# Performance work log

Measured on AMD Instinct MI355X. Metric: run time of the kernel, lower is better.

## Reference

```python
import jax, jax.numpy as jnp
import numpy as np


def setup_inputs() -> dict:
    key = jax.random.key(0)
    k1, k2, k3 = jax.random.split(key, 3)
    N, C_in, H, W = 32, 16, 256, 256
    C_out, K = 64, 3
    x = jax.random.normal(k1, (N, C_in, H, W), dtype=jnp.float32)
    # match nn.Conv2d default init scale roughly (values irrelevant for correctness harness)
    fan_in = C_in * K * K
    bound = 1.0 / np.sqrt(fan_in)
    conv_weight = jax.random.normal(k2, (C_out, C_in, K, K), dtype=jnp.float32) * bound
    conv_bias = jax.random.normal(k3, (C_out,), dtype=jnp.float32) * bound
    return {"x": x, "conv_weight": conv_weight, "conv_bias": conv_bias}


def reference(x, conv_weight, conv_bias):
    # Conv2d: stride=1, padding=0 (VALID), dilation=1, groups=1
    y = jax.lax.conv_general_dilated(
        x, conv_weight,
        window_strides=(1, 1), padding='VALID',
        dimension_numbers=('NCHW', 'OIHW', 'NCHW'),
    ) + conv_bias[None, :, None, None]          # (N, C_out, OH, OW)
    y = jnp.min(y, axis=1, keepdims=True)       # min over output channels -> (N, 1, OH, OW)
    return jnp.tanh(jnp.tanh(y))                # double tanh
```

## Files before the change

kernel.cpp:

```cpp
#include <hip/hip_runtime.h>
#include <hip/hip_bf16.h>

typedef __attribute__((ext_vector_type(8)))  short short8;
typedef __attribute__((ext_vector_type(4)))  float f32x4;
typedef __attribute__((ext_vector_type(16))) float f32x16;

#define CIN   16
#define HH    256
#define WW    256
#define OHH   254
#define OWW   254

#define HSTR   (36 * 8)
#define HALF   (34 * HSTR + 8)

__device__ __forceinline__ ushort f2bf(float f) {
    unsigned u = __builtin_bit_cast(unsigned, f);
    unsigned r = (u + 0x7fffu + ((u >> 16) & 1u)) >> 16;
    return (ushort)r;
}

__device__ __forceinline__ float dtanh2(float x) {
    const float K = 2.8853900817779268f;
    float xc = fminf(fmaxf(x, -9.0f), 9.0f);
    float e1 = __builtin_amdgcn_exp2f(K * xc);
    float t1 = 1.0f - 2.0f * __builtin_amdgcn_rcpf(e1 + 1.0f);
    float e2 = __builtin_amdgcn_exp2f(K * t1);
    return 1.0f - 2.0f * __builtin_amdgcn_rcpf(e2 + 1.0f);
}

__global__ void prep_weights(const float* __restrict__ wsrc, ushort* __restrict__ wfrag) {
    int idx = blockIdx.x * 256 + threadIdx.x;
    if (idx >= 9216) return;
    int r    = idx & 7;
    int lane = (idx >> 3) & 63;
    int j    = (idx >> 9) & 1;
    int tap  = idx >> 10;
    int ci   = 8 * (lane >> 5) + r;
    int co   = j * 32 + (lane & 31);
    int kh   = tap / 3, kw = tap - 3 * kh;
    wfrag[idx] = f2bf(wsrc[(co * CIN + ci) * 9 + kh * 3 + kw]);
}

__global__ __launch_bounds__(256, 4) void conv_min_tanh(
        const float* __restrict__ x, const ushort* __restrict__ wfrag,
        const float* __restrict__ bias, float* __restrict__ out) {
    __shared__ ushort lds[2 * HALF];

    const int tid = threadIdx.x;
    const int n   = blockIdx.z;
    const int oh0 = blockIdx.y * 32;
    const int ow0 = blockIdx.x * 32;
    const int HW  = HH * WW;

    const float* xb = x + (size_t)n * CIN * HW;
    auto stage_pos = [&](int pos) {
        int hp  = pos / 36;
        int r2  = pos - hp * 36;
        int ciq = r2 / 9;
        int w4  = r2 - ciq * 9;
        int hg  = min(oh0 + hp, HH - 1);
        int wg  = min(ow0 + 4 * w4, WW - 4);
        const float* src = xb + (size_t)(ciq * 4) * HW + hg * WW + wg;
        f32x4 v0 = *reinterpret_cast<const f32x4*>(src);
        f32x4 v1 = *reinterpret_cast<const f32x4*>(src + HW);
        f32x4 v2 = *reinterpret_cast<const f32x4*>(src + 2 * HW);
        f32x4 v3 = *reinterpret_cast<const f32x4*>(src + 3 * HW);
        ushort* dst = &lds[(ciq >> 1) * HALF + (hp * 36 + 4 * w4) * 8 + (ciq & 1) * 4];
#pragma unroll
        for (int e = 0; e < 4; ++e) {
            unsigned lo, hi;
            asm("v_cvt_pk_bf16_f32 %0, %1, %2" : "=v"(lo) : "v"(v0[e]), "v"(v1[e]));
            asm("v_cvt_pk_bf16_f32 %0, %1, %2" : "=v"(hi) : "v"(v2[e]), "v"(v3[e]));
            uint2 pk; pk.x = lo; pk.y = hi;
            *reinterpret_cast<uint2*>(dst + e * 8) = pk;
        }
    };
#pragma unroll
    for (int it = 0; it < 4; ++it) stage_pos(tid + it * 256);
    if (tid < 1224 - 1024) stage_pos(tid + 1024);

    const int lane  = tid & 63;
    const int wid   = tid >> 6;
    const int jw    = wid & 1;
    const int rh    = wid >> 1;
    const int px    = lane & 31;
    const int khalf = lane >> 5;

    short8 wf[9];
#pragma unroll
    for (int tap = 0; tap < 9; ++tap)
        wf[tap] = *reinterpret_cast<const short8*>(wfrag + ((tap * 2 + jw) * 64 + lane) * 8);
    f32x16 bi;
#pragma unroll
    for (int q4 = 0; q4 < 4; ++q4) {
        f32x4 b = *reinterpret_cast<const f32x4*>(bias + jw * 32 + 4 * khalf + 8 * q4);
#pragma unroll
        for (int s = 0; s < 4; ++s) bi[q4 * 4 + s] = b[s];
    }
    const ushort* bp[9];
#pragma unroll
    for (int tap = 0; tap < 9; ++tap) {
        int kh = tap / 3, kw = tap - 3 * kh;
        bp[tap] = &lds[khalf * HALF + (rh * 16 + kh) * HSTR + (px + kw) * 8];
    }

    __syncthreads();

    float mv[16];
#pragma unroll
    for (int i = 0; i < 16; ++i) {
        f32x16 a = bi;
#pragma unroll
        for (int tap = 0; tap < 9; ++tap) {
            short8 b = *reinterpret_cast<const short8*>(bp[tap] + i * HSTR);
            a = __builtin_amdgcn_mfma_f32_32x32x16_bf16(wf[tap], b, a, 0, 0, 0);
        }
        float v = a[0];
#pragma unroll
        for (int r = 1; r < 16; ++r) v = fminf(v, a[r]);
        v = fminf(v, __shfl_xor(v, 32, 64));
        mv[i] = v;
    }

    __syncthreads();

    if (lane < 32) {
#pragma unroll
        for (int i = 0; i < 16; ++i)
            lds[(jw * 32 + rh * 16 + i) * 32 + px] = f2bf(mv[i]);
    }
    __syncthreads();

    const int row = tid >> 3, px4 = (tid & 7) * 4;
    uint2 p0 = *reinterpret_cast<const uint2*>(&lds[(     row) * 32 + px4]);
    uint2 p1 = *reinterpret_cast<const uint2*>(&lds[(32 + row) * 32 + px4]);
    f32x4 y;
#pragma unroll
    for (int e = 0; e < 4; ++e) {
        unsigned w0 = (e < 2) ? p0.x : p0.y;
        unsigned w1 = (e < 2) ? p1.x : p1.y;
        float f0 = __builtin_bit_cast(float, (e & 1) ? (w0 & 0xffff0000u) : (w0 << 16));
        float f1 = __builtin_bit_cast(float, (e & 1) ? (w1 & 0xffff0000u) : (w1 << 16));
        y[e] = dtanh2(fminf(f0, f1));
    }
    const int oh = oh0 + row, ow = ow0 + px4;
    if (oh < OHH) {
        float* op = &out[((size_t)n * OHH + oh) * OWW + ow];
        if (ow + 3 < OWW) {
            *reinterpret_cast<f32x4*>(op) = y;
        } else {
#pragma unroll
            for (int e = 0; e < 4; ++e)
                if (ow + e < OWW) op[e] = y[e];
        }
    }
}

extern "C" void kernel_launch(void* const* d_in, const int* in_sizes, int n_in,
                              void* d_out, int out_size, void* d_ws, size_t ws_size,
                              hipStream_t stream) {
    const float* x = (const float*)d_in[0];
    const float* w = (const float*)d_in[1];
    const float* b = (const float*)d_in[2];
    float* out     = (float*)d_out;
    ushort* wfrag  = (ushort*)d_ws;

    prep_weights<<<36, 256, 0, stream>>>(w, wfrag);
    dim3 grid(8, 8, 32);
    conv_min_tanh<<<grid, dim3(256, 1, 1), 0, stream>>>(x, wfrag, b, out);
}
```

Baseline: 57.66 us.

## Pipeline input staging in row chunks, overlapping global loads with MFMA compute

```diff
diff --git a/kernel.cpp b/kernel.cpp
--- a/kernel.cpp
+++ b/kernel.cpp
@@ -42,19 +42,20 @@
     wfrag[idx] = f2bf(wsrc[(co * CIN + ci) * 9 + kh * 3 + kw]);
 }
 
-__global__ __launch_bounds__(256, 4) void conv_min_tanh(
+__global__ __launch_bounds__(256, 3) void conv_min_tanh(
         const float* __restrict__ x, const ushort* __restrict__ wfrag,
         const float* __restrict__ bias, float* __restrict__ out) {
     __shared__ ushort lds[2 * HALF];
+    __shared__ ushort mp[2][32][32];
 
     const int tid = threadIdx.x;
     const int n   = blockIdx.z;
     const int oh0 = blockIdx.y * 32;
     const int ow0 = blockIdx.x * 32;
     const int HW  = HH * WW;
-
     const float* xb = x + (size_t)n * CIN * HW;
-    auto stage_pos = [&](int pos) {
+
+    auto stage0 = [&](int pos) {
         int hp  = pos / 36;
         int r2  = pos - hp * 36;
         int ciq = r2 / 9;
@@ -76,14 +77,27 @@
             *reinterpret_cast<uint2*>(dst + e * 8) = pk;
         }
     };
-#pragma unroll
-    for (int it = 0; it < 4; ++it) stage_pos(tid + it * 256);
-    if (tid < 1224 - 1024) stage_pos(tid + 1024);
+    stage0(tid);
+    if (tid < 104) stage0(tid + 256);
+
+    const int lr0  = tid / 36;
+    const int rm0  = tid - lr0 * 36;
+    const int ciq0 = rm0 / 9;
+    const int w40  = rm0 - ciq0 * 9;
+    const int wg0  = min(ow0 + 4 * w40, WW - 4);
+    const int gc0  = ciq0 * 4 * HW + wg0;
+    const bool two = (tid < 32);
+    const int ciq1 = (4 + tid) / 9;
+    const int w41  = (4 + tid) - ciq1 * 9;
+    const int wg1  = min(ow0 + 4 * w41, WW - 4);
+    const int gc1  = ciq1 * 4 * HW + wg1;
+    const int ld0  = (ciq0 >> 1) * HALF + (4 * w40) * 8 + (ciq0 & 1) * 4;
+    const int ld1  = (ciq1 >> 1) * HALF + (4 * w41) * 8 + (ciq1 & 1) * 4;
 
     const int lane  = tid & 63;
     const int wid   = tid >> 6;
     const int jw    = wid & 1;
-    const int rh    = wid >> 1;
+    const int rq    = wid >> 1;
     const int px    = lane & 31;
     const int khalf = lane >> 5;
 
@@ -98,43 +112,86 @@
 #pragma unroll
         for (int s = 0; s < 4; ++s) bi[q4 * 4 + s] = b[s];
     }
-    const ushort* bp[9];
-#pragma unroll
-    for (int tap = 0; tap < 9; ++tap) {
-        int kh = tap / 3, kw = tap - 3 * kh;
-        bp[tap] = &lds[khalf * HALF + (rh * 16 + kh) * HSTR + (px + kw) * 8];
-    }
+    const ushort* bptr = &lds[khalf * HALF + (rq * 4) * HSTR + px * 8];
 
     __syncthreads();
 
-    float mv[16];
-#pragma unroll
-    for (int i = 0; i < 16; ++i) {
-        f32x16 a = bi;
-#pragma unroll
-        for (int tap = 0; tap < 9; ++tap) {
-            short8 b = *reinterpret_cast<const short8*>(bp[tap] + i * HSTR);
-            a = __builtin_amdgcn_mfma_f32_32x32x16_bf16(wf[tap], b, a, 0, 0, 0);
-        }
-        float v = a[0];
-#pragma unroll
-        for (int r = 1; r < 16; ++r) v = fminf(v, a[r]);
-        v = fminf(v, __shfl_xor(v, 32, 64));
-        mv[i] = v;
+    f32x4 ra0, ra1, ra2, ra3, rb0, rb1, rb2, rb3;
+
+#pragma unroll
+    for (int q = 0; q < 4; ++q) {
+        if (q < 3) {
+            const int c = q + 1;
+            {
+                int hg = min(oh0 + 8 * c + 2 + lr0, HH - 1);
+                const float* s = xb + gc0 + hg * WW;
+                asm volatile("global_load_dwordx4 %0, %1, off" : "=v"(ra0) : "v"(s) : "memory");
+                asm volatile("global_load_dwordx4 %0, %1, off" : "=v"(ra1) : "v"(s + HW) : "memory");
+                asm volatile("global_load_dwordx4 %0, %1, off" : "=v"(ra2) : "v"(s + 2 * HW) : "memory");
+                asm volatile("global_load_dwordx4 %0, %1, off" : "=v"(ra3) : "v"(s + 3 * HW) : "memory");
+            }
+            if (two) {
+                int hg = min(oh0 + 8 * c + 2 + 7, HH - 1);
+                const float* s = xb + gc1 + hg * WW;
+                asm volatile("global_load_dwordx4 %0, %1, off" : "=v"(rb0) : "v"(s) : "memory");
+                asm volatile("global_load_dwordx4 %0, %1, off" : "=v"(rb1) : "v"(s + HW) : "memory");
+                asm volatile("global_load_dwordx4 %0, %1, off" : "=v"(rb2) : "v"(s + 2 * HW) : "memory");
+                asm volatile("global_load_dwordx4 %0, %1, off" : "=v"(rb3) : "v"(s + 3 * HW) : "memory");
+            }
+        }
+
+#pragma unroll
+        for (int i = 0; i < 4; ++i) {
+            f32x16 a = bi;
+#pragma unroll
+            for (int kh = 0; kh < 3; ++kh)
+#pragma unroll
+                for (int kw = 0; kw < 3; ++kw) {
+                    short8 b = *reinterpret_cast<const short8*>(
+                        bptr + (8 * q + i + kh) * HSTR + kw * 8);
+                    a = __builtin_amdgcn_mfma_f32_32x32x16_bf16(wf[kh * 3 + kw], b, a, 0, 0, 0);
+                }
+            float v = a[0];
+#pragma unroll
+            for (int r = 1; r < 16; ++r) v = fminf(v, a[r]);
+            v = fminf(v, __shfl_xor(v, 32, 64));
+            if (lane < 32) mp[jw][8 * q + rq * 4 + i][px] = f2bf(v);
+        }
+
+        if (q < 3) {
+            asm volatile("s_waitcnt vmcnt(0)" ::: "memory");
+            const int c = q + 1;
+            {
+                ushort* dst = &lds[ld0 + ((8 * c + 2 + lr0) * 36) * 8];
+#pragma unroll
+                for (int e = 0; e < 4; ++e) {
+                    unsigned lo, hi;
+                    asm("v_cvt_pk_bf16_f32 %0, %1, %2" : "=v"(lo) : "v"(ra0[e]), "v"(ra1[e]));
+                    asm("v_cvt_pk_bf16_f32 %0, %1, %2" : "=v"(hi) : "v"(ra2[e]), "v"(ra3[e]));
+                    uint2 pk; pk.x = lo; pk.y = hi;
+                    *reinterpret_cast<uint2*>(dst + e * 8) = pk;
+                }
+            }
+            if (two) {
+                ushort* dst = &lds[ld1 + ((8 * c + 2 + 7) * 36) * 8];
+#pragma unroll
+                for (int e = 0; e < 4; ++e) {
+                    unsigned lo, hi;
+                    asm("v_cvt_pk_bf16_f32 %0, %1, %2" : "=v"(lo) : "v"(rb0[e]), "v"(rb1[e]));
+                    asm("v_cvt_pk_bf16_f32 %0, %1, %2" : "=v"(hi) : "v"(rb2[e]), "v"(rb3[e]));
+                    uint2 pk; pk.x = lo; pk.y = hi;
+                    *reinterpret_cast<uint2*>(dst + e * 8) = pk;
+                }
+            }
+            __syncthreads();
+        }
     }
 
     __syncthreads();
 
-    if (lane < 32) {
-#pragma unroll
-        for (int i = 0; i < 16; ++i)
-            lds[(jw * 32 + rh * 16 + i) * 32 + px] = f2bf(mv[i]);
-    }
-    __syncthreads();
-
     const int row = tid >> 3, px4 = (tid & 7) * 4;
-    uint2 p0 = *reinterpret_cast<const uint2*>(&lds[(     row) * 32 + px4]);
-    uint2 p1 = *reinterpret_cast<const uint2*>(&lds[(32 + row) * 32 + px4]);
+    uint2 p0 = *reinterpret_cast<const uint2*>(&mp[0][row][px4]);
+    uint2 p1 = *reinterpret_cast<const uint2*>(&mp[1][row][px4]);
     f32x4 y;
 #pragma unroll
     for (int e = 0; e < 4; ++e) {
```

Result: faster. 55.15 us (-4.4%).

## Stream input rows through an LDS ring buffer with double-buffered register prefetch

Applied to the files above, without the earlier changes.

```diff
diff --git a/kernel.cpp b/kernel.cpp
--- a/kernel.cpp
+++ b/kernel.cpp
@@ -10,9 +10,10 @@
 #define WW    256
 #define OHH   254
 #define OWW   254
-
-#define HSTR   (36 * 8)
-#define HALF   (34 * HSTR + 8)
+#define HW    (HH * WW)
+
+#define SLOTU  (36 * 8)
+#define HALF_R (16 * SLOTU + 8)
 
 __device__ __forceinline__ ushort f2bf(float f) {
     unsigned u = __builtin_bit_cast(unsigned, f);
@@ -42,31 +43,31 @@
     wfrag[idx] = f2bf(wsrc[(co * CIN + ci) * 9 + kh * 3 + kw]);
 }
 
-__global__ __launch_bounds__(256, 4) void conv_min_tanh(
+__global__ __launch_bounds__(256, 2) void conv_min_tanh(
         const float* __restrict__ x, const ushort* __restrict__ wfrag,
         const float* __restrict__ bias, float* __restrict__ out) {
-    __shared__ ushort lds[2 * HALF];
-
-    const int tid = threadIdx.x;
-    const int n   = blockIdx.z;
-    const int oh0 = blockIdx.y * 32;
-    const int ow0 = blockIdx.x * 32;
-    const int HW  = HH * WW;
-
+    __shared__ ushort ring[2 * HALF_R];
+    __shared__ ushort mp[2][2][4][32];
+
+    const int tid   = threadIdx.x;
+    const int ow0   = blockIdx.x * 32;
+    const int hbase = blockIdx.y * 128;
+    const int n     = blockIdx.z;
     const float* xb = x + (size_t)n * CIN * HW;
-    auto stage_pos = [&](int pos) {
-        int hp  = pos / 36;
-        int r2  = pos - hp * 36;
-        int ciq = r2 / 9;
-        int w4  = r2 - ciq * 9;
-        int hg  = min(oh0 + hp, HH - 1);
+
+    auto stage_inline = [&](int pos) {
+        int lr  = pos / 36;
+        int rm  = pos - lr * 36;
+        int ciq = rm / 9;
+        int w4  = rm - ciq * 9;
+        int hg  = min(hbase + lr, HH - 1);
         int wg  = min(ow0 + 4 * w4, WW - 4);
         const float* src = xb + (size_t)(ciq * 4) * HW + hg * WW + wg;
         f32x4 v0 = *reinterpret_cast<const f32x4*>(src);
         f32x4 v1 = *reinterpret_cast<const f32x4*>(src + HW);
         f32x4 v2 = *reinterpret_cast<const f32x4*>(src + 2 * HW);
         f32x4 v3 = *reinterpret_cast<const f32x4*>(src + 3 * HW);
-        ushort* dst = &lds[(ciq >> 1) * HALF + (hp * 36 + 4 * w4) * 8 + (ciq & 1) * 4];
+        ushort* dst = &ring[(ciq >> 1) * HALF_R + lr * SLOTU + (4 * w4) * 8 + (ciq & 1) * 4];
 #pragma unroll
         for (int e = 0; e < 4; ++e) {
             unsigned lo, hi;
@@ -76,17 +77,53 @@
             *reinterpret_cast<uint2*>(dst + e * 8) = pk;
         }
     };
-#pragma unroll
-    for (int it = 0; it < 4; ++it) stage_pos(tid + it * 256);
-    if (tid < 1224 - 1024) stage_pos(tid + 1024);
+    stage_inline(tid);
+    if (tid < 32) stage_inline(tid + 256);
+
+    const bool sa = (tid < 144);
+    const int lr  = tid / 36;
+    const int rm  = tid - lr * 36;
+    const int ciq = rm / 9;
+    const int w4  = rm - ciq * 9;
+    const int wg  = min(ow0 + 4 * w4, WW - 4);
+    const float* gbase = xb + (size_t)(ciq * 4) * HW + wg;
+    ushort* sdst = &ring[(ciq >> 1) * HALF_R + (4 * w4) * 8 + (ciq & 1) * 4];
+
+    f32x4 ra0 = {}, ra1 = {}, ra2 = {}, ra3 = {};
+    f32x4 rb0 = {}, rb1 = {}, rb2 = {}, rb3 = {};
+
+#define ISSUE(cc, r0, r1, r2, r3)                                              \
+    if (sa) {                                                                  \
+        int hg = min(hbase + 4 * (cc) + lr, HH - 1);                           \
+        const float* s_ = gbase + hg * WW;                                     \
+        asm volatile("global_load_dwordx4 %0, %1, off" : "=v"(r0) : "v"(s_) : "memory");           \
+        asm volatile("global_load_dwordx4 %0, %1, off" : "=v"(r1) : "v"(s_ + HW) : "memory");      \
+        asm volatile("global_load_dwordx4 %0, %1, off" : "=v"(r2) : "v"(s_ + 2 * HW) : "memory");  \
+        asm volatile("global_load_dwordx4 %0, %1, off" : "=v"(r3) : "v"(s_ + 3 * HW) : "memory");  \
+    }
+
+#define WRITEBK(cc, r0, r1, r2, r3)                                            \
+    if (sa) {                                                                  \
+        ushort* d_ = sdst + ((4 * (cc) + lr) & 15) * SLOTU;                    \
+        _Pragma("unroll")                                                      \
+        for (int e = 0; e < 4; ++e) {                                          \
+            unsigned lo_, hi_;                                                 \
+            asm("v_cvt_pk_bf16_f32 %0, %1, %2" : "=v"(lo_) : "v"(r0[e]), "v"(r1[e]));  \
+            asm("v_cvt_pk_bf16_f32 %0, %1, %2" : "=v"(hi_) : "v"(r2[e]), "v"(r3[e]));  \
+            uint2 pk_; pk_.x = lo_; pk_.y = hi_;                               \
+            *reinterpret_cast<uint2*>(d_ + e * 8) = pk_;                       \
+        }                                                                      \
+    }
+
+    ISSUE(2, ra0, ra1, ra2, ra3);
+    ISSUE(3, rb0, rb1, rb2, rb3);
 
     const int lane  = tid & 63;
     const int wid   = tid >> 6;
     const int jw    = wid & 1;
-    const int rh    = wid >> 1;
+    const int rq    = wid >> 1;
     const int px    = lane & 31;
     const int khalf = lane >> 5;
-
     short8 wf[9];
 #pragma unroll
     for (int tap = 0; tap < 9; ++tap)
@@ -98,63 +135,63 @@
 #pragma unroll
         for (int s = 0; s < 4; ++s) bi[q4 * 4 + s] = b[s];
     }
-    const ushort* bp[9];
-#pragma unroll
-    for (int tap = 0; tap < 9; ++tap) {
-        int kh = tap / 3, kw = tap - 3 * kh;
-        bp[tap] = &lds[khalf * HALF + (rh * 16 + kh) * HSTR + (px + kw) * 8];
-    }
-
-    __syncthreads();
-
-    float mv[16];
-#pragma unroll
-    for (int i = 0; i < 16; ++i) {
-        f32x16 a = bi;
-#pragma unroll
-        for (int tap = 0; tap < 9; ++tap) {
-            short8 b = *reinterpret_cast<const short8*>(bp[tap] + i * HSTR);
-            a = __builtin_amdgcn_mfma_f32_32x32x16_bf16(wf[tap], b, a, 0, 0, 0);
-        }
-        float v = a[0];
-#pragma unroll
-        for (int r = 1; r < 16; ++r) v = fminf(v, a[r]);
-        v = fminf(v, __shfl_xor(v, 32, 64));
-        mv[i] = v;
-    }
-
-    __syncthreads();
-
-    if (lane < 32) {
-#pragma unroll
-        for (int i = 0; i < 16; ++i)
-            lds[(jw * 32 + rh * 16 + i) * 32 + px] = f2bf(mv[i]);
-    }
-    __syncthreads();
-
-    const int row = tid >> 3, px4 = (tid & 7) * 4;
-    uint2 p0 = *reinterpret_cast<const uint2*>(&lds[(     row) * 32 + px4]);
-    uint2 p1 = *reinterpret_cast<const uint2*>(&lds[(32 + row) * 32 + px4]);
-    f32x4 y;
-#pragma unroll
-    for (int e = 0; e < 4; ++e) {
-        unsigned w0 = (e < 2) ? p0.x : p0.y;
-        unsigned w1 = (e < 2) ? p1.x : p1.y;
-        float f0 = __builtin_bit_cast(float, (e & 1) ? (w0 & 0xffff0000u) : (w0 << 16));
-        float f1 = __builtin_bit_cast(float, (e & 1) ? (w1 & 0xffff0000u) : (w1 << 16));
-        y[e] = dtanh2(fminf(f0, f1));
-    }
-    const int oh = oh0 + row, ow = ow0 + px4;
-    if (oh < OHH) {
-        float* op = &out[((size_t)n * OHH + oh) * OWW + ow];
-        if (ow + 3 < OWW) {
-            *reinterpret_cast<f32x4*>(op) = y;
-        } else {
-#pragma unroll
-            for (int e = 0; e < 4; ++e)
-                if (ow + e < OWW) op[e] = y[e];
-        }
-    }
+    const ushort* bptr = &ring[khalf * HALF_R + px * 8];
+
+    asm volatile("s_waitcnt lgkmcnt(0)" ::: "memory");
+    __builtin_amdgcn_s_barrier();
+
+#pragma unroll 2
+    for (int c = 0; c < 32; ++c) {
+#pragma unroll
+        for (int jj = 0; jj < 2; ++jj) {
+            const int R = 4 * c + 2 * rq + jj;
+            f32x16 a = bi;
+#pragma unroll
+            for (int kh = 0; kh < 3; ++kh) {
+                const ushort* rp = bptr + ((R + kh) & 15) * SLOTU;
+#pragma unroll
+                for (int kw = 0; kw < 3; ++kw) {
+                    short8 b = *reinterpret_cast<const short8*>(rp + kw * 8);
+                    a = __builtin_amdgcn_mfma_f32_32x32x16_bf16(wf[kh * 3 + kw], b, a, 0, 0, 0);
+                }
+            }
+            float v = a[0];
+#pragma unroll
+            for (int r = 1; r < 16; ++r) v = fminf(v, a[r]);
+            v = fminf(v, __shfl_xor(v, 32, 64));
+            if (lane < 32) mp[c & 1][jw][2 * rq + jj][px] = f2bf(v);
+        }
+
+        if (c < 31) {
+            if ((c & 1) == 0) {
+                asm volatile("s_waitcnt vmcnt(4)"
+                             : "+v"(ra0), "+v"(ra1), "+v"(ra2), "+v"(ra3) :: "memory");
+                WRITEBK(c + 2, ra0, ra1, ra2, ra3);
+                ISSUE(min(c + 4, 32), ra0, ra1, ra2, ra3);
+            } else {
+                asm volatile("s_waitcnt vmcnt(4)"
+                             : "+v"(rb0), "+v"(rb1), "+v"(rb2), "+v"(rb3) :: "memory");
+                WRITEBK(c + 2, rb0, rb1, rb2, rb3);
+                ISSUE(min(c + 4, 32), rb0, rb1, rb2, rb3);
+            }
+        }
+
+        asm volatile("s_waitcnt lgkmcnt(0)" ::: "memory");
+        __builtin_amdgcn_s_barrier();
+
+        if (tid < 128) {
+            const int r4 = tid >> 5, opx = tid & 31;
+            float f0 = __builtin_bit_cast(float, (unsigned)mp[c & 1][0][r4][opx] << 16);
+            float f1 = __builtin_bit_cast(float, (unsigned)mp[c & 1][1][r4][opx] << 16);
+            float y  = dtanh2(fminf(f0, f1));
+            const int oh = hbase + 4 * c + r4;
+            const int ow = ow0 + opx;
+            if (oh < OHH && ow < OWW)
+                out[((size_t)n * OHH + oh) * OWW + ow] = y;
+        }
+    }
+#undef ISSUE
+#undef WRITEBK
 }
 
 extern "C" void kernel_launch(void* const* d_in, const int* in_sizes, int n_in,
@@ -167,6 +204,6 @@
     ushort* wfrag  = (ushort*)d_ws;
 
     prep_weights<<<36, 256, 0, stream>>>(w, wfrag);
-    dim3 grid(8, 8, 32);
+    dim3 grid(8, 2, 32);
     conv_min_tanh<<<grid, dim3(256, 1, 1), 0, stream>>>(x, wfrag, b, out);
 }
```

Measured after the change: 51.85 us. 10.1% less time.
